# Performance work log

Hardware: AMD Instinct MI355X
Metric: run time of the kernel (lower is better)

## Reference

```python
import jax, jax.numpy as jnp
import numpy as np

# geometry constants from init_kwargs
VX, VY, VZ = 0.1, 0.1, 4.0
X_OFF, Y_OFF, Z_OFF = VX / 2 - 51.2, VY / 2 - 51.2, VZ / 2 - 3.0
GY, GX = 1024, 1024  # round((51.2-(-51.2))/0.1)
NUM_BEV = 8
BN_EPS = 1e-3


def setup_inputs() -> dict:
    key = jax.random.key(0)
    k1, k2, k3, k4, k5, k6 = jax.random.split(key, 6)
    N, P, C_in, C_out = 40000, 32, 10, 64
    voxel_features = jax.random.normal(k1, (N, P, 4), jnp.float32)
    voxel_num_points = jax.random.randint(k2, (N,), 1, P + 1, jnp.int32)
    bb = jax.random.randint(k3, (N,), 0, 2, jnp.int32)
    yy = jax.random.randint(k4, (N,), 0, GY, jnp.int32)
    xx = jax.random.randint(k5, (N,), 0, GX, jnp.int32)
    coords = jnp.stack([bb, jnp.zeros((N,), jnp.int32), yy, xx], axis=1)
    record_len = jnp.array([N // 2, N - N // 2], jnp.int32)
    W = jax.random.normal(k6, (C_in, C_out), jnp.float32) * 0.1
    gamma = jnp.ones((C_out,), jnp.float32)
    beta = jnp.zeros((C_out,), jnp.float32)
    run_mean = jnp.zeros((C_out,), jnp.float32)
    run_var = jnp.ones((C_out,), jnp.float32)
    return {"voxel_features": voxel_features, "W": W, "gamma": gamma,
            "beta": beta, "run_mean": run_mean, "run_var": run_var,
            "voxel_num_points": voxel_num_points, "coords": coords,
            "record_len": record_len}


def reference(voxel_features, W, gamma, beta, run_mean, run_var,
              voxel_num_points, coords, record_len):
    N, P, _ = voxel_features.shape
    npts = voxel_num_points.astype(voxel_features.dtype)  # [N]
    xyz = voxel_features[:, :, :3]

    # cluster offset feature
    points_mean = xyz.sum(axis=1, keepdims=True) / npts[:, None, None]
    f_cluster = xyz - points_mean

    # pillar-center offset feature
    cx = coords[:, 3].astype(voxel_features.dtype)[:, None] * VX + X_OFF
    cy = coords[:, 2].astype(voxel_features.dtype)[:, None] * VY + Y_OFF
    cz = coords[:, 1].astype(voxel_features.dtype)[:, None] * VZ + Z_OFF
    f_center = jnp.stack([xyz[:, :, 0] - cx, xyz[:, :, 1] - cy,
                          xyz[:, :, 2] - cz], axis=-1)

    features = jnp.concatenate([voxel_features, f_cluster, f_center], axis=-1)  # [N,P,10]

    # padding mask
    mask = (voxel_num_points[:, None] > jnp.arange(P, dtype=jnp.int32)[None, :])
    mask = mask[..., None].astype(voxel_features.dtype)  # [N,P,1]
    features = features * mask

    # PFN layer: Linear(10->64, no bias) + BN(eval) + ReLU + max over points
    x = jnp.einsum('npc,cd->npd', features, W)  # [N,P,64]
    x = (x - run_mean) * jax.lax.rsqrt(run_var + BN_EPS) * gamma + beta
    x = jax.nn.relu(x)
    pillar_features = x.max(axis=1)  # [N,64]

    # hand-crafted BEV stats
    safe_n = jnp.clip(npts, 1.0)[:, None]  # [N,1]
    num_points_norm = npts[:, None] / P
    intensity = voxel_features[:, :, 3:4]
    mean_intensity = (intensity * mask).sum(axis=1) / safe_n
    z = xyz[:, :, 2:3]
    mean_height = (z * mask).sum(axis=1) / safe_n
    max_height = (z * mask + (1 - mask) * -1e6).max(axis=1)
    min_height = (z * mask + (1 - mask) * 1e6).min(axis=1)
    height_span = max_height - min_height
    pm = (xyz * mask).sum(axis=1, keepdims=True) / safe_n[:, :, None]
    var_xyz = (((xyz - pm) ** 2) * mask).sum(axis=1) / safe_n  # [N,3]
    pillar_bev = jnp.concatenate([num_points_norm, mean_intensity, mean_height,
                                  max_height, height_span, var_xyz[:, 0:1],
                                  var_xyz[:, 1:2], var_xyz[:, 2:3]], axis=1)  # [N,8]

    batch_size = record_len.shape[0]
    b = jnp.clip(coords[:, 0], 0, batch_size - 1)
    y_idx = coords[:, 2]
    x_idx = coords[:, 3]
    vox_bev = jnp.zeros((batch_size, NUM_BEV, GY, GX), voxel_features.dtype)
    vox_bev = vox_bev.at[b, :, y_idx, x_idx].set(pillar_bev)

    return pillar_features, vox_bev
```

## Files before the change

kernel.cpp:

```cpp
#include <hip/hip_runtime.h>

#define GYD 1024
#define GXD 1024
#define NUM_BEV 8

__device__ __forceinline__ float rdlanef(float x, int l) {
    return __int_as_float(__builtin_amdgcn_readlane(__float_as_int(x), l));
}
template <int CTRL, int ROWMASK>
__device__ __forceinline__ float dppf(float x, float oldv) {
    return __int_as_float(__builtin_amdgcn_update_dpp(
        __float_as_int(oldv), __float_as_int(x), CTRL, ROWMASK, 0xF, false));
}
__device__ __forceinline__ float dsum32(float x) {
    x += dppf<0x111, 0xF>(x, 0.f);
    x += dppf<0x112, 0xF>(x, 0.f);
    x += dppf<0x114, 0xF>(x, 0.f);
    x += dppf<0x118, 0xF>(x, 0.f);
    x += dppf<0x142, 0xA>(x, 0.f);
    return x;
}
__device__ __forceinline__ float dmax32(float x) {
    x = fmaxf(x, dppf<0x111, 0xF>(x, x));
    x = fmaxf(x, dppf<0x112, 0xF>(x, x));
    x = fmaxf(x, dppf<0x114, 0xF>(x, x));
    x = fmaxf(x, dppf<0x118, 0xF>(x, x));
    x = fmaxf(x, dppf<0x142, 0xA>(x, x));
    return x;
}
__device__ __forceinline__ float dmin32(float x) {
    x = fminf(x, dppf<0x111, 0xF>(x, x));
    x = fminf(x, dppf<0x112, 0xF>(x, x));
    x = fminf(x, dppf<0x114, 0xF>(x, x));
    x = fminf(x, dppf<0x118, 0xF>(x, x));
    x = fminf(x, dppf<0x142, 0xA>(x, x));
    return x;
}

__global__ __launch_bounds__(256) void pillar_kernel(
    const float4* __restrict__ vf,
    const float* __restrict__ W,
    const float* __restrict__ gammap, const float* __restrict__ betap,
    const float* __restrict__ rmeanp, const float* __restrict__ rvarp,
    const int* __restrict__ npts_arr,
    const int* __restrict__ coords,
    float* __restrict__ pillar_out,
    float* __restrict__ bev_vals,
    int* __restrict__ winner,
    int N, int bs)
{
    const int wid  = threadIdx.x >> 6;
    const int lane = threadIdx.x & 63;
    const int half = lane >> 5;
    const int sl   = lane & 31;
    const int n0   = blockIdx.x * 8 + wid * 2;
    const int n    = n0 + half;
    const bool valid = (n < N);
    const int nn = valid ? n : 0;

    const int d = lane;
    const float w0 = W[d],       w1 = W[64 + d],  w2 = W[128 + d], w3 = W[192 + d];
    const float w4 = W[256 + d], w5 = W[320 + d], w6 = W[384 + d];
    const float w7 = W[448 + d], w8 = W[512 + d], w9 = W[576 + d];
    const float g  = gammap[d], bt = betap[d], rm = rmeanp[d], rv = rvarp[d];

    const int npts = npts_arr[nn];
    const int4 crd = ((const int4*)coords)[nn];
    const float cx = (float)crd.w * 0.1f - 51.15f;
    const float cy = (float)crd.z * 0.1f - 51.15f;
    const float cz = (float)crd.y * 4.0f - 1.0f;

    float4 v = make_float4(0.f, 0.f, 0.f, 0.f);
    if (valid) v = vf[(size_t)nn * 32 + sl];
    const bool pv = sl < npts;
    const float m = pv ? 1.f : 0.f;

    const float sx   = dsum32(v.x);
    const float sy   = dsum32(v.y);
    const float sz   = dsum32(v.z);
    const float smx  = dsum32(v.x * m);
    const float smy  = dsum32(v.y * m);
    const float smz  = dsum32(v.z * m);
    const float smI  = dsum32(v.w * m);
    const float sx2  = dsum32(v.x * v.x * m);
    const float sy2  = dsum32(v.y * v.y * m);
    const float sz2  = dsum32(v.z * v.z * m);
    const float maxz = dmax32(pv ? v.z : -1e6f);
    const float minz = dmin32(pv ? v.z :  1e6f);

    const float scale = g * rsqrtf(rv + 1e-3f);
    const float shift = fmaf(-rm, scale, bt);
    const float A = (w0 + w4 + w7) * scale;
    const float B = (w1 + w5 + w8) * scale;
    const float C = (w2 + w6 + w9) * scale;
    const float D = w3 * scale;

#pragma unroll
    for (int h = 0; h < 2; ++h) {
        const int L  = h << 5;
        const int nh = __builtin_amdgcn_readlane(npts, L);
        const float invnh = 1.f / (float)nh;
        const float mx = rdlanef(sx, L + 31) * invnh;
        const float my = rdlanef(sy, L + 31) * invnh;
        const float mz = rdlanef(sz, L + 31) * invnh;
        const float cxh = rdlanef(cx, L), cyh = rdlanef(cy, L), czh = rdlanef(cz, L);
        const float E   = -(mx * w4 + my * w5 + mz * w6 + cxh * w7 + cyh * w8 + czh * w9);
        const float bse = fmaf(E, scale, shift);

        float acc = -1e30f;
        for (int p = 0; p < nh; ++p) {
            const float qx = rdlanef(v.x, L + p);
            const float qy = rdlanef(v.y, L + p);
            const float qz = rdlanef(v.z, L + p);
            const float qw = rdlanef(v.w, L + p);
            acc = fmaxf(acc, fmaf(qx, A, fmaf(qy, B, fmaf(qz, C, fmaf(qw, D, bse)))));
        }
        if (nh < 32) acc = fmaxf(acc, shift);
        acc = fmaxf(acc, 0.f);
        const int np_ = n0 + h;
        if (np_ < N) pillar_out[(size_t)np_ * 64 + lane] = acc;
    }

    if (valid && sl == 31) {
        const float fn = (float)npts, invn = 1.f / fn;
        const float pmx = smx * invn, pmy = smy * invn, pmz = smz * invn;
        const float vvx = fmaf(-pmx, pmx, sx2 * invn);
        const float vvy = fmaf(-pmy, pmy, sy2 * invn);
        const float vvz = fmaf(-pmz, pmz, sz2 * invn);
        float4* bvp = (float4*)&bev_vals[(size_t)n * 8];
        bvp[0] = make_float4(fn * (1.f / 32.f), smI * invn, pmz, maxz);
        bvp[1] = make_float4(maxz - minz, vvx, vvy, vvz);
        const int b = crd.x < 0 ? 0 : (crd.x > bs - 1 ? bs - 1 : crd.x);
        atomicMax(&winner[(b * GYD + crd.z) * GXD + crd.w], n + 1);
    }
}

__global__ __launch_bounds__(256) void bev_fill(
    const int4* __restrict__ winner4,
    const float* __restrict__ bev_vals,
    float* __restrict__ vox_bev, int bs)
{
    const int gidx = blockIdx.x * 256 + threadIdx.x;
    const int4 w = winner4[gidx];
    const int c0 = gidx << 2;
    const int b  = c0 >> 20;
    const int yx = c0 & ((1 << 20) - 1);
    float* basep = vox_bev + (((size_t)b * NUM_BEV) << 20) + yx;
    if ((w.x | w.y | w.z | w.w) == 0) {
        const float4 z4 = make_float4(0.f, 0.f, 0.f, 0.f);
#pragma unroll
        for (int k = 0; k < NUM_BEV; ++k)
            *(float4*)(basep + ((size_t)k << 20)) = z4;
    } else {
#pragma unroll
        for (int k = 0; k < NUM_BEV; ++k) {
            float4 o;
            o.x = (w.x > 0) ? bev_vals[(size_t)(w.x - 1) * 8 + k] : 0.f;
            o.y = (w.y > 0) ? bev_vals[(size_t)(w.y - 1) * 8 + k] : 0.f;
            o.z = (w.z > 0) ? bev_vals[(size_t)(w.z - 1) * 8 + k] : 0.f;
            o.w = (w.w > 0) ? bev_vals[(size_t)(w.w - 1) * 8 + k] : 0.f;
            *(float4*)(basep + ((size_t)k << 20)) = o;
        }
    }
}

extern "C" void kernel_launch(void* const* d_in, const int* in_sizes, int n_in,
                              void* d_out, int out_size, void* d_ws, size_t ws_size,
                              hipStream_t stream) {
    const float4* vf    = (const float4*)d_in[0];
    const float* W      = (const float*)d_in[1];
    const float* gammap = (const float*)d_in[2];
    const float* betap  = (const float*)d_in[3];
    const float* rmeanp = (const float*)d_in[4];
    const float* rvarp  = (const float*)d_in[5];
    const int* npts     = (const int*)d_in[6];
    const int* coords   = (const int*)d_in[7];
    const int N  = in_sizes[6];
    const int bs = in_sizes[8];

    float* pillar_out = (float*)d_out;
    float* vox_bev    = (float*)d_out + (size_t)N * 64;

    int* winner     = (int*)d_ws;
    float* bev_vals = (float*)((char*)d_ws + (size_t)bs * GYD * GXD * sizeof(int));

    hipMemsetAsync(winner, 0, (size_t)bs * GYD * GXD * sizeof(int), stream);

    const int blocksA = (N + 7) / 8;
    pillar_kernel<<<blocksA, 256, 0, stream>>>(vf, W, gammap, betap, rmeanp, rvarp,
                                               npts, coords, pillar_out, bev_vals,
                                               winner, N, bs);
    const int blocksB = (bs << 20) / (256 * 4);
    bev_fill<<<blocksB, 256, 0, stream>>>((const int4*)winner, bev_vals, vox_bev, bs);
}
```

Baseline: 142.5 us.

## Process both pillars per wave concurrently via LDS point staging and float2 channels

Points are staged in shared memory so that each half-wave handles its own pillar, and each lane computes two output channels as float2. The two halves no longer run their point loops one after the other using readlane broadcasts. Padded slots are filled with point 0 so the loop can run to the larger point count of the two pillars without changing the max. This halves the serial loop work per wave, in exchange for LDS traffic and more registers.

```diff
diff --git a/kernel.cpp b/kernel.cpp
--- a/kernel.cpp
+++ b/kernel.cpp
@@ -35,6 +35,16 @@
     x = fminf(x, dppf<0x118, 0xF>(x, x));
     x = fminf(x, dppf<0x142, 0xA>(x, x));
     return x;
+}
+
+__device__ __forceinline__ float2 f2(float a)            { return make_float2(a, a); }
+__device__ __forceinline__ float2 add2(float2 a, float2 b){ return make_float2(a.x+b.x, a.y+b.y); }
+__device__ __forceinline__ float2 mul2(float2 a, float2 b){ return make_float2(a.x*b.x, a.y*b.y); }
+__device__ __forceinline__ float2 fma2(float2 a, float2 b, float2 c){
+    return make_float2(fmaf(a.x,b.x,c.x), fmaf(a.y,b.y,c.y));
+}
+__device__ __forceinline__ float2 max2(float2 a, float2 b){
+    return make_float2(fmaxf(a.x,b.x), fmaxf(a.y,b.y));
 }
 
 __global__ __launch_bounds__(256) void pillar_kernel(
@@ -49,6 +59,7 @@
     int* __restrict__ winner,
     int N, int bs)
 {
+    __shared__ float4 pts[4][2][32];
     const int wid  = threadIdx.x >> 6;
     const int lane = threadIdx.x & 63;
     const int half = lane >> 5;
@@ -58,11 +69,15 @@
     const bool valid = (n < N);
     const int nn = valid ? n : 0;
 
-    const int d = lane;
-    const float w0 = W[d],       w1 = W[64 + d],  w2 = W[128 + d], w3 = W[192 + d];
-    const float w4 = W[256 + d], w5 = W[320 + d], w6 = W[384 + d];
-    const float w7 = W[448 + d], w8 = W[512 + d], w9 = W[576 + d];
-    const float g  = gammap[d], bt = betap[d], rm = rmeanp[d], rv = rvarp[d];
+    const int c0 = sl, c1 = sl + 32;
+    float2 w_[10];
+#pragma unroll
+    for (int k = 0; k < 10; ++k)
+        w_[k] = make_float2(W[k * 64 + c0], W[k * 64 + c1]);
+    const float2 gg = make_float2(gammap[c0], gammap[c1]);
+    const float2 bb = make_float2(betap[c0],  betap[c1]);
+    const float2 rmn= make_float2(rmeanp[c0], rmeanp[c1]);
+    const float2 rvr= make_float2(rvarp[c0],  rvarp[c1]);
 
     const int npts = npts_arr[nn];
     const int4 crd = ((const int4*)coords)[nn];
@@ -74,6 +89,10 @@
     if (valid) v = vf[(size_t)nn * 32 + sl];
     const bool pv = sl < npts;
     const float m = pv ? 1.f : 0.f;
+
+    pts[wid][half][sl] = v;
+    const float4 p0 = pts[wid][half][0];
+    if (!pv) pts[wid][half][sl] = p0;
 
     const float sx   = dsum32(v.x);
     const float sy   = dsum32(v.y);
@@ -88,41 +107,47 @@
     const float maxz = dmax32(pv ? v.z : -1e6f);
     const float minz = dmin32(pv ? v.z :  1e6f);
 
-    const float scale = g * rsqrtf(rv + 1e-3f);
-    const float shift = fmaf(-rm, scale, bt);
-    const float A = (w0 + w4 + w7) * scale;
-    const float B = (w1 + w5 + w8) * scale;
-    const float C = (w2 + w6 + w9) * scale;
-    const float D = w3 * scale;
-
-#pragma unroll
-    for (int h = 0; h < 2; ++h) {
-        const int L  = h << 5;
-        const int nh = __builtin_amdgcn_readlane(npts, L);
-        const float invnh = 1.f / (float)nh;
-        const float mx = rdlanef(sx, L + 31) * invnh;
-        const float my = rdlanef(sy, L + 31) * invnh;
-        const float mz = rdlanef(sz, L + 31) * invnh;
-        const float cxh = rdlanef(cx, L), cyh = rdlanef(cy, L), czh = rdlanef(cz, L);
-        const float E   = -(mx * w4 + my * w5 + mz * w6 + cxh * w7 + cyh * w8 + czh * w9);
-        const float bse = fmaf(E, scale, shift);
-
-        float acc = -1e30f;
-        for (int p = 0; p < nh; ++p) {
-            const float qx = rdlanef(v.x, L + p);
-            const float qy = rdlanef(v.y, L + p);
-            const float qz = rdlanef(v.z, L + p);
-            const float qw = rdlanef(v.w, L + p);
-            acc = fmaxf(acc, fmaf(qx, A, fmaf(qy, B, fmaf(qz, C, fmaf(qw, D, bse)))));
-        }
-        if (nh < 32) acc = fmaxf(acc, shift);
-        acc = fmaxf(acc, 0.f);
-        const int np_ = n0 + h;
-        if (np_ < N) pillar_out[(size_t)np_ * 64 + lane] = acc;
+    const float invn = 1.f / (float)npts;
+    const float mx = (half ? rdlanef(sx, 63) : rdlanef(sx, 31)) * invn;
+    const float my = (half ? rdlanef(sy, 63) : rdlanef(sy, 31)) * invn;
+    const float mz = (half ? rdlanef(sz, 63) : rdlanef(sz, 31)) * invn;
+
+    const int nA = __builtin_amdgcn_readlane(npts, 0);
+    const int nB = __builtin_amdgcn_readlane(npts, 32);
+    const int nmax = nA > nB ? nA : nB;
+
+    const float2 scale = mul2(gg, make_float2(rsqrtf(rvr.x + 1e-3f), rsqrtf(rvr.y + 1e-3f)));
+    const float2 shift = fma2(f2(-1.f), mul2(rmn, scale), bb);
+    const float2 A = mul2(add2(add2(w_[0], w_[4]), w_[7]), scale);
+    const float2 B = mul2(add2(add2(w_[1], w_[5]), w_[8]), scale);
+    const float2 C = mul2(add2(add2(w_[2], w_[6]), w_[9]), scale);
+    const float2 D = mul2(w_[3], scale);
+    float2 E = mul2(f2(mx), w_[4]);
+    E = fma2(f2(my), w_[5], E);
+    E = fma2(f2(mz), w_[6], E);
+    E = fma2(f2(cx), w_[7], E);
+    E = fma2(f2(cy), w_[8], E);
+    E = fma2(f2(cz), w_[9], E);
+    const float2 bse = fma2(f2(-1.f), mul2(E, scale), shift);
+
+    float2 acc = make_float2(-1e30f, -1e30f);
+#pragma unroll 2
+    for (int p = 0; p < nmax; ++p) {
+        const float4 q = pts[wid][half][p];
+        const float2 t = fma2(f2(q.x), A, fma2(f2(q.y), B,
+                         fma2(f2(q.z), C, fma2(f2(q.w), D, bse))));
+        acc = max2(acc, t);
+    }
+    if (npts < 32) acc = max2(acc, shift);
+    acc = max2(acc, f2(0.f));
+
+    if (valid) {
+        pillar_out[(size_t)n * 64 + c0] = acc.x;
+        pillar_out[(size_t)n * 64 + c1] = acc.y;
     }
 
     if (valid && sl == 31) {
-        const float fn = (float)npts, invn = 1.f / fn;
+        const float fn = (float)npts;
         const float pmx = smx * invn, pmy = smy * invn, pmz = smz * invn;
         const float vvx = fmaf(-pmx, pmx, sx2 * invn);
         const float vvy = fmaf(-pmy, pmy, sy2 * invn);
```

Result: faster. 130.5 us (-8.4%).
